# Kernel optimization log

Hardware: AMD Instinct MI355X
Metric: run time of the kernel (lower is better)

Reference implementation:

```python
import jax, jax.numpy as jnp
import numpy as np

ALPHA = 0.2  # LeakyReLU negative slope
NEG = -9e15

def _gat_head(Wh, a1, a2, adj_mask):
    # Wh: [N,O], a1/a2: [O], adj_mask: [N,N] bool
    e = jax.nn.leaky_relu(jnp.einsum('no,o->n', Wh, a1)[:, None]
                          + jnp.einsum('no,o->n', Wh, a2)[None, :], ALPHA)
    att = jax.nn.softmax(jnp.where(adj_mask, e, NEG), axis=-1)
    return att @ Wh  # [N,O]

def setup_inputs() -> dict:
    key = jax.random.key(0)
    ks = jax.random.split(key, 6)
    N, F_IN, O, H, C = 4096, 512, 64, 8, 16
    x = jax.random.normal(ks[0], (N, F_IN), jnp.float32)
    adj = jax.random.randint(ks[1], (N, N), 0, 2, jnp.int32)
    W = jax.random.normal(ks[2], (H, F_IN, O), jnp.float32) * 0.05
    a = jax.random.normal(ks[3], (H, 2 * O), jnp.float32) * 0.05
    W_out = jax.random.normal(ks[4], (H * O, C), jnp.float32) * 0.05
    a_out = jax.random.normal(ks[5], (2 * C,), jnp.float32) * 0.05
    return {'x': x, 'adj': adj, 'W': W, 'a': a, 'W_out': W_out, 'a_out': a_out}

def reference(x, adj, W, a, W_out, a_out):
    N = x.shape[0]
    H, _, O = W.shape
    C = W_out.shape[1]
    mask = adj > 0  # [N,N]
    # multi-head attention layer (vmapped over heads)
    Wh = jnp.einsum('nf,hfo->hno', x, W)  # [H,N,O]
    a1, a2 = a[:, :O], a[:, O:]
    h_heads = jax.vmap(_gat_head, in_axes=(0, 0, 0, None))(Wh, a1, a2, mask)  # [H,N,O]
    h = jax.nn.elu(h_heads)  # concat=True -> elu per head
    h = jnp.transpose(h, (1, 0, 2)).reshape(N, H * O)  # concat heads
    # output attention layer (concat=False)
    Wh_o = h @ W_out  # [N,C]
    out = _gat_head(Wh_o, a_out[:C], a_out[C:], mask)  # [N,C]
    out = jax.nn.elu(out)
    return jax.nn.log_softmax(out, axis=1)
```

## Files before the change

kernel.cpp:

```cpp
#include <hip/hip_runtime.h>


typedef __attribute__((ext_vector_type(8))) short short8;
typedef __attribute__((ext_vector_type(4))) float f32x4;
typedef unsigned long long u64;
typedef unsigned short u16;
typedef unsigned int u32;

__device__ __forceinline__ u16 f2bf_rne(float f){
  u32 u = __float_as_uint(f);
  return (u16)((u + 0x7fffu + ((u >> 16) & 1u)) >> 16);
}
__device__ __forceinline__ void async16(void* lds, const void* g){
  __builtin_amdgcn_global_load_lds((const __attribute__((address_space(1))) u32*)g,
                                   (__attribute__((address_space(3))) u32*)lds, 16, 0, 0);
}
__device__ __forceinline__ void async4(void* lds, const void* g){
  __builtin_amdgcn_global_load_lds((const __attribute__((address_space(1))) u32*)g,
                                   (__attribute__((address_space(3))) u32*)lds, 4, 0, 0);
}

__global__ __launch_bounds__(256) void k_prep(const float* __restrict__ x,
                                              const float* __restrict__ W,
                                              const int* __restrict__ adj,
                                              u16* __restrict__ xA,
                                              u16* __restrict__ wB,
                                              u64* __restrict__ bits_t){
  int lane = threadIdx.x & 63;
  if (blockIdx.x < 1024){
    int t = blockIdx.x * 256 + threadIdx.x;
    int n = t & 4095, fg = t >> 12;
    const float* src = x + (size_t)n * 512 + fg * 8;
    float4 v0 = ((const float4*)src)[0];
    float4 v1 = ((const float4*)src)[1];
    u32 pk[4];
    pk[0] = f2bf_rne(v0.x) | ((u32)f2bf_rne(v0.y) << 16);
    pk[1] = f2bf_rne(v0.z) | ((u32)f2bf_rne(v0.w) << 16);
    pk[2] = f2bf_rne(v1.x) | ((u32)f2bf_rne(v1.y) << 16);
    pk[3] = f2bf_rne(v1.z) | ((u32)f2bf_rne(v1.w) << 16);
    *(uint4*)(xA + ((size_t)fg * 4096 + n) * 8) = *(uint4*)pk;
  } else if (blockIdx.x < 1152){
    int t = (blockIdx.x - 1024) * 256 + threadIdx.x;
    int o = t & 63, fg = (t >> 6) & 63, h = t >> 12;
    const float* src = W + ((size_t)h * 512 + fg * 8) * 64 + o;
    u32 pk[4];
    #pragma unroll
    for (int p = 0; p < 4; ++p){
      u16 lo = f2bf_rne(src[(2 * p) * 64]);
      u16 hi = f2bf_rne(src[(2 * p + 1) * 64]);
      pk[p] = lo | ((u32)hi << 16);
    }
    *(uint4*)(wB + (size_t)h * 32768 + ((size_t)fg * 64 + o) * 8) = *(uint4*)pk;
  } else {
    int Wd = (blockIdx.x - 1152) * 4 + (threadIdx.x >> 6);
    int jg = Wd >> 5;
    int i0 = (Wd & 31) * 128;
    const int* base = adj + (size_t)jg * 64 + lane;
    #pragma unroll 1
    for (int u = 0; u < 32; ++u){
      int ib = i0 + u * 4;
      int v0 = base[(size_t)(ib + 0) * 4096];
      int v1 = base[(size_t)(ib + 1) * 4096];
      int v2 = base[(size_t)(ib + 2) * 4096];
      int v3 = base[(size_t)(ib + 3) * 4096];
      u64 m0 = __ballot(v0 != 0);
      u64 m1 = __ballot(v1 != 0);
      u64 m2 = __ballot(v2 != 0);
      u64 m3 = __ballot(v3 != 0);
      if (lane == 0){
        u64* d = bits_t + (size_t)jg * 4096 + ib;
        d[0] = m0; d[1] = m1; d[2] = m2; d[3] = m3;
      }
    }
  }
}

__global__ __launch_bounds__(256) void k_gemm1(const u16* __restrict__ xA,
                                               const u16* __restrict__ wB,
                                               const float* __restrict__ av,
                                               u16* __restrict__ whB,
                                               float* __restrict__ e11, float* __restrict__ e102,
                                               float* __restrict__ e21, float* __restrict__ e202){
  __shared__ u16 tr[4096];
  int h    = blockIdx.y;
  int nblk = blockIdx.x;
  int lane = threadIdx.x & 63;
  int wv   = threadIdx.x >> 6;
  int row16 = lane & 15, grp = lane >> 4;
  int n0 = nblk * 64;
  int n0w = n0 + wv * 16;
  const u16* wBh = wB + (size_t)h * 32768;
  f32x4 acc[4] = {};
  #pragma unroll 4
  for (int ks = 0; ks < 16; ++ks){
    int fgb = ks * 4 + grp;
    short8 af = *(const short8*)(xA + ((size_t)fgb * 4096 + n0w + row16) * 8);
    #pragma unroll
    for (int nt = 0; nt < 4; ++nt){
      short8 bf = *(const short8*)(wBh + ((size_t)fgb * 64 + nt * 16 + row16) * 8);
      acc[nt] = __builtin_amdgcn_mfma_f32_16x16x32_bf16(af, bf, acc[nt], 0, 0, 0);
    }
  }
  float a1v[4], a2v[4];
  #pragma unroll
  for (int nt = 0; nt < 4; ++nt){
    a1v[nt] = av[h * 128 + nt * 16 + row16];
    a2v[nt] = av[h * 128 + 64 + nt * 16 + row16];
  }
  #pragma unroll
  for (int r = 0; r < 4; ++r){
    float p1 = acc[0][r]*a1v[0] + acc[1][r]*a1v[1] + acc[2][r]*a1v[2] + acc[3][r]*a1v[3];
    float p2 = acc[0][r]*a2v[0] + acc[1][r]*a2v[1] + acc[2][r]*a2v[2] + acc[3][r]*a2v[3];
    #pragma unroll
    for (int d = 1; d < 16; d <<= 1){ p1 += __shfl_xor(p1, d, 64); p2 += __shfl_xor(p2, d, 64); }
    if (row16 == 0){
      int idx = h * 4096 + n0w + grp * 4 + r;
      e11[idx] = __expf(p1); e102[idx] = __expf(0.2f * p1);
      e21[idx] = __expf(p2); e202[idx] = __expf(0.2f * p2);
    }
  }
  #pragma unroll
  for (int nt = 0; nt < 4; ++nt)
    #pragma unroll
    for (int r = 0; r < 4; ++r){
      int jl = wv * 16 + grp * 4 + r;
      int o  = nt * 16 + row16;
      tr[((jl >> 3) * 64 + o) * 8 + (jl & 7)] = f2bf_rne(acc[nt][r]);
    }
  __syncthreads();
  u16* dst = whB + (size_t)h * 262144 + (size_t)n0 * 64;
  #pragma unroll
  for (int q = 0; q < 2; ++q)
    *(uint4*)(dst + (threadIdx.x * 2 + q) * 8) = *(const uint4*)(tr + (threadIdx.x * 2 + q) * 8);
}

__global__ __launch_bounds__(256) void k_att1(const u16* __restrict__ whB,
                                              const u64* __restrict__ bits_t,
                                              const float* __restrict__ e11, const float* __restrict__ e102,
                                              const float* __restrict__ e21, const float* __restrict__ e202,
                                              u16* __restrict__ pnum, float* __restrict__ pden){
  __shared__ u16  smB[2][4096];
  __shared__ float smT[2][2][64];
  __shared__ u32  smLut[4];
  int h     = blockIdx.y;
  int iblk  = blockIdx.x;
  int split = blockIdx.z;
  int lane = threadIdx.x & 63;
  int wv   = threadIdx.x >> 6;
  int row16 = lane & 15, grp = lane >> 4;
  if (threadIdx.x < 4)
    smLut[threadIdx.x] = ((threadIdx.x & 1) ? 0xFFFFu : 0u) | ((threadIdx.x & 2) ? 0xFFFF0000u : 0u);
  int i = iblk * 64 + wv * 16 + row16;
  int hoff = h * 4096;
  float f1  = e11[hoff + i];
  float f02 = e102[hoff + i];
  const u16* whBh = whB + (size_t)h * 262144;
  int jbeg = split * 1024;

  short8 bden;
  #pragma unroll
  for (int t = 0; t < 8; ++t) bden[t] = (row16 == 0) ? (short)0x3F80 : (short)0;

  auto stage = [&](int bb, int j0){
    const char* g = (const char*)whBh + (size_t)j0 * 128 + wv * 2048 + lane * 16;
    char* l = (char*)(&smB[bb][0]) + wv * 2048;
    async16(l, g);
    async16(l + 1024, g + 1024);
    if (wv == 0)      async4(&smT[bb][0][0], (const char*)(e21  + hoff + j0) + lane * 4);
    else if (wv == 1) async4(&smT[bb][1][0], (const char*)(e202 + hoff + j0) + lane * 4);
  };

  f32x4 acc[4] = {};
  f32x4 accden = {};
  stage(0, jbeg);
  for (int c = 0; c < 16; ++c){
    int bb = c & 1;
    u64 mrow = bits_t[(size_t)(split * 16 + c) * 4096 + i];
    __syncthreads();
    if (c < 15) stage(bb ^ 1, jbeg + (c + 1) * 64);
    #pragma unroll
    for (int ks = 0; ks < 2; ++ks){
      int kb = ks * 32 + grp * 8;
      float4 eA = *(const float4*)(&smT[bb][0][kb]);
      float4 eB = *(const float4*)(&smT[bb][0][kb + 4]);
      float4 gA = *(const float4*)(&smT[bb][1][kb]);
      float4 gB = *(const float4*)(&smT[bb][1][kb + 4]);
      float e1v[8] = {eA.x, eA.y, eA.z, eA.w, eB.x, eB.y, eB.z, eB.w};
      float e2v[8] = {gA.x, gA.y, gA.z, gA.w, gB.x, gB.y, gB.z, gB.w};
      const u16* bbase = &smB[bb][(ks * 4 + grp) * 512];
      short8 bf0 = *(const short8*)(bbase + (0 * 16 + row16) * 8);
      short8 bf1 = *(const short8*)(bbase + (1 * 16 + row16) * 8);
      short8 bf2 = *(const short8*)(bbase + (2 * 16 + row16) * 8);
      short8 bf3 = *(const short8*)(bbase + (3 * 16 + row16) * 8);
      u32 mb = ((u32)(mrow >> (ks * 32)) >> (grp * 8)) & 0xffu;
      u32 pk[4];
      #pragma unroll
      for (int t2i = 0; t2i < 4; ++t2i){
        float w0 = fmaxf(f1 * e1v[2 * t2i],     f02 * e2v[2 * t2i]);
        float w1 = fmaxf(f1 * e1v[2 * t2i + 1], f02 * e2v[2 * t2i + 1]);
        u32 p = __builtin_amdgcn_perm(__float_as_uint(w1), __float_as_uint(w0), 0x07060302u);
        pk[t2i] = p & smLut[(mb >> (2 * t2i)) & 3u];
      }
      short8 af = *(short8*)pk;
      acc[0] = __builtin_amdgcn_mfma_f32_16x16x32_bf16(af, bf0, acc[0], 0, 0, 0);
      acc[1] = __builtin_amdgcn_mfma_f32_16x16x32_bf16(af, bf1, acc[1], 0, 0, 0);
      acc[2] = __builtin_amdgcn_mfma_f32_16x16x32_bf16(af, bf2, acc[2], 0, 0, 0);
      acc[3] = __builtin_amdgcn_mfma_f32_16x16x32_bf16(af, bf3, acc[3], 0, 0, 0);
      accden = __builtin_amdgcn_mfma_f32_16x16x32_bf16(af, bden, accden, 0, 0, 0);
    }
  }

  #pragma unroll
  for (int r = 0; r < 4; ++r){
    int n = iblk * 64 + wv * 16 + grp * 4 + r;
    if (row16 == 0)
      pden[((size_t)split * 8 + h) * 4096 + n] = accden[r];
    u16* dst = pnum + ((size_t)split * 4096 + n) * 512 + h * 64 + row16;
    #pragma unroll
    for (int nt = 0; nt < 4; ++nt)
      dst[nt * 16] = f2bf_rne(acc[nt][r]);
  }
}

__global__ __launch_bounds__(256) void k_gemm2(const u16* __restrict__ pnum,
                                               const float* __restrict__ pden,
                                               const float* __restrict__ Wout,
                                               const float* __restrict__ aout,
                                               u16* __restrict__ whoB,
                                               float* __restrict__ e11o, float* __restrict__ e102o,
                                               float* __restrict__ e21o, float* __restrict__ e202o){
  __shared__ float Wl[8192];
  __shared__ float hrow[16 * 516];
  __shared__ float sden[128];
  int n0 = blockIdx.x * 16;
  for (int t = threadIdx.x; t < 8192; t += 256) Wl[t] = Wout[t];
  if (threadIdx.x < 128){
    int hh = threadIdx.x >> 4, nn = threadIdx.x & 15;
    float d = 0.f;
    #pragma unroll
    for (int s = 0; s < 4; ++s) d += pden[((size_t)s * 8 + hh) * 4096 + n0 + nn];
    sden[threadIdx.x] = d;
  }
  __syncthreads();
  {
    int nn = threadIdx.x >> 4;
    int fc = threadIdx.x & 15;
    int f0 = fc * 32;
    int hh = fc >> 1;
    float dinv = 1.f / sden[hh * 16 + nn];
    float v[32];
    #pragma unroll
    for (int k = 0; k < 32; ++k) v[k] = 0.f;
    #pragma unroll
    for (int s = 0; s < 4; ++s){
      const u16* p = pnum + ((size_t)s * 4096 + n0 + nn) * 512 + f0;
      #pragma unroll
      for (int q = 0; q < 4; ++q){
        uint4 raw = *(const uint4*)(p + q * 8);
        u32 rw[4] = {raw.x, raw.y, raw.z, raw.w};
        #pragma unroll
        for (int d2 = 0; d2 < 4; ++d2){
          v[q * 8 + d2 * 2]     += __uint_as_float(rw[d2] << 16);
          v[q * 8 + d2 * 2 + 1] += __uint_as_float(rw[d2] & 0xffff0000u);
        }
      }
    }
    #pragma unroll
    for (int k = 0; k < 32; ++k){
      float val = v[k] * dinv;
      val = val > 0.f ? val : (__expf(val) - 1.f);
      hrow[nn * 516 + f0 + k] = val;
    }
  }
  __syncthreads();
  int c  = threadIdx.x & 15;
  int rl = threadIdx.x >> 4;
  int n = n0 + rl;
  const float4* hr = (const float4*)(hrow + rl * 516);
  float acc = 0.f;
  #pragma unroll 8
  for (int f4 = 0; f4 < 128; ++f4){
    float4 hv = hr[f4];
    int f = f4 * 4;
    acc += hv.x * Wl[f * 16 + c] + hv.y * Wl[(f + 1) * 16 + c]
         + hv.z * Wl[(f + 2) * 16 + c] + hv.w * Wl[(f + 3) * 16 + c];
  }
  whoB[((size_t)(n >> 3) * 16 + c) * 8 + (n & 7)] = f2bf_rne(acc);
  float p1 = acc * aout[c], p2 = acc * aout[16 + c];
  #pragma unroll
  for (int d = 1; d < 16; d <<= 1){ p1 += __shfl_xor(p1, d, 64); p2 += __shfl_xor(p2, d, 64); }
  if (c == 0){
    e11o[n] = __expf(p1); e102o[n] = __expf(0.2f * p1);
    e21o[n] = __expf(p2); e202o[n] = __expf(0.2f * p2);
  }
}

__global__ __launch_bounds__(256) void k_att2(const u16* __restrict__ whoB,
                                              const u64* __restrict__ bits_t,
                                              const float* __restrict__ e11o, const float* __restrict__ e102o,
                                              const float* __restrict__ e21o, const float* __restrict__ e202o,
                                              float* __restrict__ pnum, float* __restrict__ pden){
  __shared__ u32 smLut[4];
  int iblk  = blockIdx.x;
  int split = blockIdx.y;
  int lane = threadIdx.x & 63;
  int wv   = threadIdx.x >> 6;
  int row16 = lane & 15, grp = lane >> 4;
  if (threadIdx.x < 4)
    smLut[threadIdx.x] = ((threadIdx.x & 1) ? 0xFFFFu : 0u) | ((threadIdx.x & 2) ? 0xFFFF0000u : 0u);
  __syncthreads();
  int i = iblk * 64 + wv * 16 + row16;
  float f1  = e11o[i];
  float f02 = e102o[i];
  int jbeg = split * 256;
  short8 bden;
  #pragma unroll
  for (int t = 0; t < 8; ++t) bden[t] = (row16 == 0) ? (short)0x3F80 : (short)0;

  f32x4 acc = {};
  f32x4 accden = {};
  #pragma unroll
  for (int c = 0; c < 4; ++c){
    int j0 = jbeg + c * 64;
    u64 mrow = bits_t[(size_t)(split * 4 + c) * 4096 + i];
    #pragma unroll
    for (int ks = 0; ks < 2; ++ks){
      int sb = (j0 >> 3) + ks * 4 + grp;
      short8 bf = *(const short8*)(whoB + ((size_t)sb * 16 + row16) * 8);
      const float* t1 = e21o  + j0 + ks * 32 + grp * 8;
      const float* t2 = e202o + j0 + ks * 32 + grp * 8;
      float4 eA = *(const float4*)t1;
      float4 eB = *(const float4*)(t1 + 4);
      float4 gA = *(const float4*)t2;
      float4 gB = *(const float4*)(t2 + 4);
      float e1v[8] = {eA.x, eA.y, eA.z, eA.w, eB.x, eB.y, eB.z, eB.w};
      float e2v[8] = {gA.x, gA.y, gA.z, gA.w, gB.x, gB.y, gB.z, gB.w};
      u32 mb = ((u32)(mrow >> (ks * 32)) >> (grp * 8)) & 0xffu;
      u32 pk[4];
      #pragma unroll
      for (int t2i = 0; t2i < 4; ++t2i){
        float w0 = fmaxf(f1 * e1v[2 * t2i],     f02 * e2v[2 * t2i]);
        float w1 = fmaxf(f1 * e1v[2 * t2i + 1], f02 * e2v[2 * t2i + 1]);
        u32 p = __builtin_amdgcn_perm(__float_as_uint(w1), __float_as_uint(w0), 0x07060302u);
        pk[t2i] = p & smLut[(mb >> (2 * t2i)) & 3u];
      }
      short8 af = *(short8*)pk;
      acc    = __builtin_amdgcn_mfma_f32_16x16x32_bf16(af, bf, acc, 0, 0, 0);
      accden = __builtin_amdgcn_mfma_f32_16x16x32_bf16(af, bden, accden, 0, 0, 0);
    }
  }
  #pragma unroll
  for (int r = 0; r < 4; ++r){
    int n = iblk * 64 + wv * 16 + grp * 4 + r;
    if (row16 == 0)
      pden[(size_t)n * 16 + split] = accden[r];
    pnum[((size_t)n * 16 + split) * 16 + row16] = acc[r];
  }
}

__global__ __launch_bounds__(256) void k_final(const float* __restrict__ pnum,
                                               const float* __restrict__ pden,
                                               float* __restrict__ out){
  int tid = blockIdx.x * 256 + threadIdx.x;
  int c = tid & 15;
  int n = tid >> 4;
  float num = 0.f, den = 0.f;
  #pragma unroll
  for (int s = 0; s < 16; ++s){
    num += pnum[((size_t)n * 16 + s) * 16 + c];
    den += pden[(size_t)n * 16 + s];
  }
  float v = num / den;
  v = v > 0.f ? v : (__expf(v) - 1.f);
  float m = v;
  #pragma unroll
  for (int d = 1; d < 16; d <<= 1) m = fmaxf(m, __shfl_xor(m, d, 64));
  float es = __expf(v - m), ss = es;
  #pragma unroll
  for (int d = 1; d < 16; d <<= 1) ss += __shfl_xor(ss, d, 64);
  out[(size_t)n * 16 + c] = v - m - __logf(ss);
}

extern "C" void kernel_launch(void* const* d_in, const int* in_sizes, int n_in,
                              void* d_out, int out_size, void* d_ws, size_t ws_size,
                              hipStream_t stream){
  (void)in_sizes; (void)n_in; (void)out_size; (void)ws_size;
  const float* x    = (const float*)d_in[0];
  const int*   adj  = (const int*)d_in[1];
  const float* W    = (const float*)d_in[2];
  const float* av   = (const float*)d_in[3];
  const float* Wout = (const float*)d_in[4];
  const float* aout = (const float*)d_in[5];
  float* out = (float*)d_out;
  char* ws = (char*)d_ws;

  u64*  bits_t  = (u64*)(ws + 0x0000000);
  u16*  whB     = (u16*)(ws + 0x0200000);
  float* e11    = (float*)(ws + 0x0600000);
  float* e102   = (float*)(ws + 0x0620000);
  float* e21    = (float*)(ws + 0x0640000);
  float* e202   = (float*)(ws + 0x0660000);
  u16*  xA      = (u16*)(ws + 0x0680000);
  u16*  wB      = (u16*)(ws + 0x0A80000);
  u16*  pnum1   = (u16*)(ws + 0x0680000);
  float* pden1  = (float*)(ws + 0x1680000);
  u16*  whoB    = (u16*)(ws + 0x1700000);
  float* e11o   = (float*)(ws + 0x1720000);
  float* e102o  = (float*)(ws + 0x1724000);
  float* e21o   = (float*)(ws + 0x1728000);
  float* e202o  = (float*)(ws + 0x172C000);
  float* pnum2  = (float*)(ws + 0x1730000);
  float* pden2  = (float*)(ws + 0x1B30000);

  k_prep<<<dim3(1664), dim3(256), 0, stream>>>(x, W, adj, xA, wB, bits_t);
  k_gemm1<<<dim3(64, 8), dim3(256), 0, stream>>>(xA, wB, av, whB, e11, e102, e21, e202);
  k_att1<<<dim3(64, 8, 4), dim3(256), 0, stream>>>(whB, bits_t, e11, e102, e21, e202, pnum1, pden1);
  k_gemm2<<<dim3(256), dim3(256), 0, stream>>>(pnum1, pden1, Wout, aout, whoB, e11o, e102o, e21o, e202o);
  k_att2<<<dim3(64, 16), dim3(256), 0, stream>>>(whoB, bits_t, e11o, e102o, e21o, e202o, pnum2, pden2);
  k_final<<<dim3(256), dim3(256), 0, stream>>>(pnum2, pden2, out);
}
```

Measured before the change: 191.7 us.

## Fuse prep/gemm1 and gemm2/att2/final into persistent kernels with grid barriers

Merges the prep and first projection GEMM into one 1024-block kernel, and the second projection, output attention and final log-softmax into another. The stages are separated by a software two-level atomic grid barrier, which replaces five launches with two plus a memset. The adjacency bit-packing is remapped so that each wave reads contiguous rows. gemm2 now runs on 4 rows per block with a split-K reduction and reads Wout from global memory instead of LDS. The grid barrier depends on all 1024 blocks being co-resident (launch_bounds 256,4 over 256 CUs), so the code can deadlock if occupancy falls short.

```diff
diff --git a/kernel.cpp b/kernel.cpp
--- a/kernel.cpp
+++ b/kernel.cpp
@@ -20,15 +20,50 @@
                                    (__attribute__((address_space(3))) u32*)lds, 4, 0, 0);
 }
 
-__global__ __launch_bounds__(256) void k_prep(const float* __restrict__ x,
-                                              const float* __restrict__ W,
-                                              const int* __restrict__ adj,
-                                              u16* __restrict__ xA,
-                                              u16* __restrict__ wB,
-                                              u64* __restrict__ bits_t){
-  int lane = threadIdx.x & 63;
-  if (blockIdx.x < 1024){
-    int t = blockIdx.x * 256 + threadIdx.x;
+__device__ __forceinline__ void grid_barrier(u32* bar){
+  __syncthreads();
+  if (threadIdx.x == 0){
+    u32* gen  = bar;
+    u32* root = bar + 32;
+    u32* leaf = bar + 64 + (blockIdx.x & 31) * 32;
+    u32 mygen = __hip_atomic_load(gen, __ATOMIC_RELAXED, __HIP_MEMORY_SCOPE_AGENT);
+    __threadfence();
+    u32 o = __hip_atomic_fetch_add(leaf, 1u, __ATOMIC_RELAXED, __HIP_MEMORY_SCOPE_AGENT);
+    if (o == 31u){
+      __hip_atomic_store(leaf, 0u, __ATOMIC_RELAXED, __HIP_MEMORY_SCOPE_AGENT);
+      u32 r = __hip_atomic_fetch_add(root, 1u, __ATOMIC_RELAXED, __HIP_MEMORY_SCOPE_AGENT);
+      if (r == 31u){
+        __hip_atomic_store(root, 0u, __ATOMIC_RELAXED, __HIP_MEMORY_SCOPE_AGENT);
+        __threadfence();
+        __hip_atomic_fetch_add(gen, 1u, __ATOMIC_RELEASE, __HIP_MEMORY_SCOPE_AGENT);
+      } else {
+        while (__hip_atomic_load(gen, __ATOMIC_RELAXED, __HIP_MEMORY_SCOPE_AGENT) == mygen)
+          __builtin_amdgcn_s_sleep(16);
+      }
+    } else {
+      while (__hip_atomic_load(gen, __ATOMIC_RELAXED, __HIP_MEMORY_SCOPE_AGENT) == mygen)
+        __builtin_amdgcn_s_sleep(16);
+    }
+    __threadfence();
+  }
+  __syncthreads();
+}
+
+__global__ __launch_bounds__(256, 4) void k_gat_a(
+    const float* __restrict__ x, const float* __restrict__ W,
+    const int* __restrict__ adj, const float* __restrict__ av,
+    u16* __restrict__ xA, u16* __restrict__ wB, u64* __restrict__ bits_t,
+    u16* __restrict__ whB,
+    float* __restrict__ e11, float* __restrict__ e102,
+    float* __restrict__ e21, float* __restrict__ e202, u32* bar)
+{
+  __shared__ u16 tr[4096];
+  const int tid = threadIdx.x, b = blockIdx.x;
+  const int lane = tid & 63, wv = tid >> 6;
+  const int row16 = lane & 15, grp = lane >> 4;
+
+  {
+    int t = b * 256 + tid;
     int n = t & 4095, fg = t >> 12;
     const float* src = x + (size_t)n * 512 + fg * 8;
     float4 v0 = ((const float4*)src)[0];
@@ -39,8 +74,9 @@
     pk[2] = f2bf_rne(v1.x) | ((u32)f2bf_rne(v1.y) << 16);
     pk[3] = f2bf_rne(v1.z) | ((u32)f2bf_rne(v1.w) << 16);
     *(uint4*)(xA + ((size_t)fg * 4096 + n) * 8) = *(uint4*)pk;
-  } else if (blockIdx.x < 1152){
-    int t = (blockIdx.x - 1024) * 256 + threadIdx.x;
+  }
+  if (b < 128){
+    int t = b * 256 + tid;
     int o = t & 63, fg = (t >> 6) & 63, h = t >> 12;
     const float* src = W + ((size_t)h * 512 + fg * 8) * 64 + o;
     u32 pk[4];
@@ -51,87 +87,67 @@
       pk[p] = lo | ((u32)hi << 16);
     }
     *(uint4*)(wB + (size_t)h * 32768 + ((size_t)fg * 64 + o) * 8) = *(uint4*)pk;
-  } else {
-    int Wd = (blockIdx.x - 1152) * 4 + (threadIdx.x >> 6);
-    int jg = Wd >> 5;
-    int i0 = (Wd & 31) * 128;
-    const int* base = adj + (size_t)jg * 64 + lane;
-    #pragma unroll 1
-    for (int u = 0; u < 32; ++u){
-      int ib = i0 + u * 4;
-      int v0 = base[(size_t)(ib + 0) * 4096];
-      int v1 = base[(size_t)(ib + 1) * 4096];
-      int v2 = base[(size_t)(ib + 2) * 4096];
-      int v3 = base[(size_t)(ib + 3) * 4096];
-      u64 m0 = __ballot(v0 != 0);
-      u64 m1 = __ballot(v1 != 0);
-      u64 m2 = __ballot(v2 != 0);
-      u64 m3 = __ballot(v3 != 0);
-      if (lane == 0){
-        u64* d = bits_t + (size_t)jg * 4096 + ib;
-        d[0] = m0; d[1] = m1; d[2] = m2; d[3] = m3;
-      }
-    }
-  }
-}
-
-__global__ __launch_bounds__(256) void k_gemm1(const u16* __restrict__ xA,
-                                               const u16* __restrict__ wB,
-                                               const float* __restrict__ av,
-                                               u16* __restrict__ whB,
-                                               float* __restrict__ e11, float* __restrict__ e102,
-                                               float* __restrict__ e21, float* __restrict__ e202){
-  __shared__ u16 tr[4096];
-  int h    = blockIdx.y;
-  int nblk = blockIdx.x;
-  int lane = threadIdx.x & 63;
-  int wv   = threadIdx.x >> 6;
-  int row16 = lane & 15, grp = lane >> 4;
-  int n0 = nblk * 64;
-  int n0w = n0 + wv * 16;
-  const u16* wBh = wB + (size_t)h * 32768;
-  f32x4 acc[4] = {};
-  #pragma unroll 4
-  for (int ks = 0; ks < 16; ++ks){
-    int fgb = ks * 4 + grp;
-    short8 af = *(const short8*)(xA + ((size_t)fgb * 4096 + n0w + row16) * 8);
+  }
+  {
+    int w = b * 4 + wv;
+    #pragma unroll 4
+    for (int k = 0; k < 64; ++k){
+      int uid = w + k * 4096;
+      int i = uid >> 6, jg = uid & 63;
+      int v = adj[(size_t)i * 4096 + (jg << 6) + lane];
+      u64 m = __ballot(v != 0);
+      if (lane == 0) bits_t[(size_t)jg * 4096 + i] = m;
+    }
+  }
+  grid_barrier(bar);
+
+  if (b < 512){
+    int h = b >> 6, nblk = b & 63;
+    int n0 = nblk * 64, n0w = n0 + wv * 16;
+    const u16* wBh = wB + (size_t)h * 32768;
+    f32x4 acc[4] = {};
+    #pragma unroll 4
+    for (int ks = 0; ks < 16; ++ks){
+      int fgb = ks * 4 + grp;
+      short8 af = *(const short8*)(xA + ((size_t)fgb * 4096 + n0w + row16) * 8);
+      #pragma unroll
+      for (int nt = 0; nt < 4; ++nt){
+        short8 bf = *(const short8*)(wBh + ((size_t)fgb * 64 + nt * 16 + row16) * 8);
+        acc[nt] = __builtin_amdgcn_mfma_f32_16x16x32_bf16(af, bf, acc[nt], 0, 0, 0);
+      }
+    }
+    float a1v[4], a2v[4];
     #pragma unroll
     for (int nt = 0; nt < 4; ++nt){
-      short8 bf = *(const short8*)(wBh + ((size_t)fgb * 64 + nt * 16 + row16) * 8);
-      acc[nt] = __builtin_amdgcn_mfma_f32_16x16x32_bf16(af, bf, acc[nt], 0, 0, 0);
-    }
-  }
-  float a1v[4], a2v[4];
-  #pragma unroll
-  for (int nt = 0; nt < 4; ++nt){
-    a1v[nt] = av[h * 128 + nt * 16 + row16];
-    a2v[nt] = av[h * 128 + 64 + nt * 16 + row16];
-  }
-  #pragma unroll
-  for (int r = 0; r < 4; ++r){
-    float p1 = acc[0][r]*a1v[0] + acc[1][r]*a1v[1] + acc[2][r]*a1v[2] + acc[3][r]*a1v[3];
-    float p2 = acc[0][r]*a2v[0] + acc[1][r]*a2v[1] + acc[2][r]*a2v[2] + acc[3][r]*a2v[3];
-    #pragma unroll
-    for (int d = 1; d < 16; d <<= 1){ p1 += __shfl_xor(p1, d, 64); p2 += __shfl_xor(p2, d, 64); }
-    if (row16 == 0){
-      int idx = h * 4096 + n0w + grp * 4 + r;
-      e11[idx] = __expf(p1); e102[idx] = __expf(0.2f * p1);
-      e21[idx] = __expf(p2); e202[idx] = __expf(0.2f * p2);
-    }
-  }
-  #pragma unroll
-  for (int nt = 0; nt < 4; ++nt)
+      a1v[nt] = av[h * 128 + nt * 16 + row16];
+      a2v[nt] = av[h * 128 + 64 + nt * 16 + row16];
+    }
     #pragma unroll
     for (int r = 0; r < 4; ++r){
-      int jl = wv * 16 + grp * 4 + r;
-      int o  = nt * 16 + row16;
-      tr[((jl >> 3) * 64 + o) * 8 + (jl & 7)] = f2bf_rne(acc[nt][r]);
-    }
-  __syncthreads();
-  u16* dst = whB + (size_t)h * 262144 + (size_t)n0 * 64;
-  #pragma unroll
-  for (int q = 0; q < 2; ++q)
-    *(uint4*)(dst + (threadIdx.x * 2 + q) * 8) = *(const uint4*)(tr + (threadIdx.x * 2 + q) * 8);
+      float p1 = acc[0][r]*a1v[0] + acc[1][r]*a1v[1] + acc[2][r]*a1v[2] + acc[3][r]*a1v[3];
+      float p2 = acc[0][r]*a2v[0] + acc[1][r]*a2v[1] + acc[2][r]*a2v[2] + acc[3][r]*a2v[3];
+      #pragma unroll
+      for (int d = 1; d < 16; d <<= 1){ p1 += __shfl_xor(p1, d, 64); p2 += __shfl_xor(p2, d, 64); }
+      if (row16 == 0){
+        int idx = h * 4096 + n0w + grp * 4 + r;
+        e11[idx] = __expf(p1); e102[idx] = __expf(0.2f * p1);
+        e21[idx] = __expf(p2); e202[idx] = __expf(0.2f * p2);
+      }
+    }
+    #pragma unroll
+    for (int nt = 0; nt < 4; ++nt)
+      #pragma unroll
+      for (int r = 0; r < 4; ++r){
+        int jl = wv * 16 + grp * 4 + r;
+        int o  = nt * 16 + row16;
+        tr[((jl >> 3) * 64 + o) * 8 + (jl & 7)] = f2bf_rne(acc[nt][r]);
+      }
+    __syncthreads();
+    u16* dst = whB + (size_t)h * 262144 + (size_t)n0 * 64;
+    #pragma unroll
+    for (int q = 0; q < 2; ++q)
+      *(uint4*)(dst + (tid * 2 + q) * 8) = *(const uint4*)(tr + (tid * 2 + q) * 8);
+  }
 }
 
 __global__ __launch_bounds__(256) void k_att1(const u16* __restrict__ whB,
@@ -222,163 +238,162 @@
   }
 }
 
-__global__ __launch_bounds__(256) void k_gemm2(const u16* __restrict__ pnum,
-                                               const float* __restrict__ pden,
-                                               const float* __restrict__ Wout,
-                                               const float* __restrict__ aout,
-                                               u16* __restrict__ whoB,
-                                               float* __restrict__ e11o, float* __restrict__ e102o,
-                                               float* __restrict__ e21o, float* __restrict__ e202o){
-  __shared__ float Wl[8192];
-  __shared__ float hrow[16 * 516];
-  __shared__ float sden[128];
-  int n0 = blockIdx.x * 16;
-  for (int t = threadIdx.x; t < 8192; t += 256) Wl[t] = Wout[t];
-  if (threadIdx.x < 128){
-    int hh = threadIdx.x >> 4, nn = threadIdx.x & 15;
-    float d = 0.f;
-    #pragma unroll
-    for (int s = 0; s < 4; ++s) d += pden[((size_t)s * 8 + hh) * 4096 + n0 + nn];
-    sden[threadIdx.x] = d;
-  }
-  __syncthreads();
+__global__ __launch_bounds__(256, 4) void k_gat_c(
+    const u16* __restrict__ pnum1, const float* __restrict__ pden1,
+    const float* __restrict__ Wout, const float* __restrict__ aout,
+    const u64* __restrict__ bits_t,
+    u16* __restrict__ whoB,
+    float* __restrict__ e11o, float* __restrict__ e102o,
+    float* __restrict__ e21o, float* __restrict__ e202o,
+    float* __restrict__ pnum2, float* __restrict__ pden2,
+    float* __restrict__ out, u32* bar)
+{
+  __shared__ __align__(16) char smem[10496];
+  float* s_hrow = (float*)smem;
+  float* s_red  = (float*)(smem + 8320);
+  float* s_den  = (float*)(smem + 9344);
+  u32*   s_lut  = (u32*)(smem + 10240);
+  const int tid = threadIdx.x, b = blockIdx.x;
+  const int lane = tid & 63, wv = tid >> 6;
+  const int row16 = lane & 15, grp = lane >> 4;
+
+  if (tid < 4)
+    s_lut[tid] = ((tid & 1) ? 0xFFFFu : 0u) | ((tid & 2) ? 0xFFFF0000u : 0u);
+
   {
-    int nn = threadIdx.x >> 4;
-    int fc = threadIdx.x & 15;
-    int f0 = fc * 32;
-    int hh = fc >> 1;
-    float dinv = 1.f / sden[hh * 16 + nn];
-    float v[32];
-    #pragma unroll
-    for (int k = 0; k < 32; ++k) v[k] = 0.f;
-    #pragma unroll
-    for (int s = 0; s < 4; ++s){
-      const u16* p = pnum + ((size_t)s * 4096 + n0 + nn) * 512 + f0;
-      #pragma unroll
-      for (int q = 0; q < 4; ++q){
-        uint4 raw = *(const uint4*)(p + q * 8);
+    int n0 = b * 4;
+    if (tid < 32){
+      int hh = tid >> 2, nn = tid & 3;
+      float d = 0.f;
+      #pragma unroll
+      for (int s = 0; s < 4; ++s) d += pden1[((size_t)s * 8 + hh) * 4096 + n0 + nn];
+      s_den[tid] = d;
+    }
+    __syncthreads();
+    {
+      int nn = tid >> 6;
+      int fo = (tid & 63) * 8;
+      int hh = fo >> 6;
+      float dinv = 1.f / s_den[hh * 4 + nn];
+      float v[8] = {0.f,0.f,0.f,0.f,0.f,0.f,0.f,0.f};
+      #pragma unroll
+      for (int s = 0; s < 4; ++s){
+        uint4 raw = *(const uint4*)(pnum1 + ((size_t)s * 4096 + n0 + nn) * 512 + fo);
         u32 rw[4] = {raw.x, raw.y, raw.z, raw.w};
         #pragma unroll
         for (int d2 = 0; d2 < 4; ++d2){
-          v[q * 8 + d2 * 2]     += __uint_as_float(rw[d2] << 16);
-          v[q * 8 + d2 * 2 + 1] += __uint_as_float(rw[d2] & 0xffff0000u);
+          v[d2 * 2]     += __uint_as_float(rw[d2] << 16);
+          v[d2 * 2 + 1] += __uint_as_float(rw[d2] & 0xffff0000u);
         }
       }
-    }
-    #pragma unroll
-    for (int k = 0; k < 32; ++k){
-      float val = v[k] * dinv;
-      val = val > 0.f ? val : (__expf(val) - 1.f);
-      hrow[nn * 516 + f0 + k] = val;
-    }
-  }
-  __syncthreads();
-  int c  = threadIdx.x & 15;
-  int rl = threadIdx.x >> 4;
-  int n = n0 + rl;
-  const float4* hr = (const float4*)(hrow + rl * 516);
-  float acc = 0.f;
-  #pragma unroll 8
-  for (int f4 = 0; f4 < 128; ++f4){
-    float4 hv = hr[f4];
-    int f = f4 * 4;
-    acc += hv.x * Wl[f * 16 + c] + hv.y * Wl[(f + 1) * 16 + c]
-         + hv.z * Wl[(f + 2) * 16 + c] + hv.w * Wl[(f + 3) * 16 + c];
-  }
-  whoB[((size_t)(n >> 3) * 16 + c) * 8 + (n & 7)] = f2bf_rne(acc);
-  float p1 = acc * aout[c], p2 = acc * aout[16 + c];
-  #pragma unroll
-  for (int d = 1; d < 16; d <<= 1){ p1 += __shfl_xor(p1, d, 64); p2 += __shfl_xor(p2, d, 64); }
-  if (c == 0){
-    e11o[n] = __expf(p1); e102o[n] = __expf(0.2f * p1);
-    e21o[n] = __expf(p2); e202o[n] = __expf(0.2f * p2);
-  }
-}
-
-__global__ __launch_bounds__(256) void k_att2(const u16* __restrict__ whoB,
-                                              const u64* __restrict__ bits_t,
-                                              const float* __restrict__ e11o, const float* __restrict__ e102o,
-                                              const float* __restrict__ e21o, const float* __restrict__ e202o,
-                                              float* __restrict__ pnum, float* __restrict__ pden){
-  __shared__ u32 smLut[4];
-  int iblk  = blockIdx.x;
-  int split = blockIdx.y;
-  int lane = threadIdx.x & 63;
-  int wv   = threadIdx.x >> 6;
-  int row16 = lane & 15, grp = lane >> 4;
-  if (threadIdx.x < 4)
-    smLut[threadIdx.x] = ((threadIdx.x & 1) ? 0xFFFFu : 0u) | ((threadIdx.x & 2) ? 0xFFFF0000u : 0u);
-  __syncthreads();
-  int i = iblk * 64 + wv * 16 + row16;
-  float f1  = e11o[i];
-  float f02 = e102o[i];
-  int jbeg = split * 256;
-  short8 bden;
-  #pragma unroll
-  for (int t = 0; t < 8; ++t) bden[t] = (row16 == 0) ? (short)0x3F80 : (short)0;
-
-  f32x4 acc = {};
-  f32x4 accden = {};
-  #pragma unroll
-  for (int c = 0; c < 4; ++c){
-    int j0 = jbeg + c * 64;
-    u64 mrow = bits_t[(size_t)(split * 4 + c) * 4096 + i];
-    #pragma unroll
-    for (int ks = 0; ks < 2; ++ks){
-      int sb = (j0 >> 3) + ks * 4 + grp;
-      short8 bf = *(const short8*)(whoB + ((size_t)sb * 16 + row16) * 8);
-      const float* t1 = e21o  + j0 + ks * 32 + grp * 8;
-      const float* t2 = e202o + j0 + ks * 32 + grp * 8;
-      float4 eA = *(const float4*)t1;
-      float4 eB = *(const float4*)(t1 + 4);
-      float4 gA = *(const float4*)t2;
-      float4 gB = *(const float4*)(t2 + 4);
-      float e1v[8] = {eA.x, eA.y, eA.z, eA.w, eB.x, eB.y, eB.z, eB.w};
-      float e2v[8] = {gA.x, gA.y, gA.z, gA.w, gB.x, gB.y, gB.z, gB.w};
-      u32 mb = ((u32)(mrow >> (ks * 32)) >> (grp * 8)) & 0xffu;
-      u32 pk[4];
-      #pragma unroll
-      for (int t2i = 0; t2i < 4; ++t2i){
-        float w0 = fmaxf(f1 * e1v[2 * t2i],     f02 * e2v[2 * t2i]);
-        float w1 = fmaxf(f1 * e1v[2 * t2i + 1], f02 * e2v[2 * t2i + 1]);
-        u32 p = __builtin_amdgcn_perm(__float_as_uint(w1), __float_as_uint(w0), 0x07060302u);
-        pk[t2i] = p & smLut[(mb >> (2 * t2i)) & 3u];
-      }
-      short8 af = *(short8*)pk;
-      acc    = __builtin_amdgcn_mfma_f32_16x16x32_bf16(af, bf, acc, 0, 0, 0);
-      accden = __builtin_amdgcn_mfma_f32_16x16x32_bf16(af, bden, accden, 0, 0, 0);
-    }
-  }
-  #pragma unroll
-  for (int r = 0; r < 4; ++r){
-    int n = iblk * 64 + wv * 16 + grp * 4 + r;
-    if (row16 == 0)
-      pden[(size_t)n * 16 + split] = accden[r];
-    pnum[((size_t)n * 16 + split) * 16 + row16] = acc[r];
-  }
-}
-
-__global__ __launch_bounds__(256) void k_final(const float* __restrict__ pnum,
-                                               const float* __restrict__ pden,
-                                               float* __restrict__ out){
-  int tid = blockIdx.x * 256 + threadIdx.x;
-  int c = tid & 15;
-  int n = tid >> 4;
-  float num = 0.f, den = 0.f;
-  #pragma unroll
-  for (int s = 0; s < 16; ++s){
-    num += pnum[((size_t)n * 16 + s) * 16 + c];
-    den += pden[(size_t)n * 16 + s];
-  }
-  float v = num / den;
-  v = v > 0.f ? v : (__expf(v) - 1.f);
-  float m = v;
-  #pragma unroll
-  for (int d = 1; d < 16; d <<= 1) m = fmaxf(m, __shfl_xor(m, d, 64));
-  float es = __expf(v - m), ss = es;
-  #pragma unroll
-  for (int d = 1; d < 16; d <<= 1) ss += __shfl_xor(ss, d, 64);
-  out[(size_t)n * 16 + c] = v - m - __logf(ss);
+      #pragma unroll
+      for (int j = 0; j < 8; ++j){
+        float val = v[j] * dinv;
+        val = val > 0.f ? val : (__expf(val) - 1.f);
+        s_hrow[nn * 520 + fo + j] = val;
+      }
+    }
+    __syncthreads();
+    {
+      int c = tid & 15, rl = (tid >> 4) & 3, ks = tid >> 6;
+      float acc = 0.f;
+      #pragma unroll 8
+      for (int f4 = 0; f4 < 32; ++f4){
+        int f = ks * 128 + f4 * 4;
+        float4 hv = *(const float4*)(s_hrow + rl * 520 + f);
+        acc += hv.x * Wout[f * 16 + c] + hv.y * Wout[(f + 1) * 16 + c]
+             + hv.z * Wout[(f + 2) * 16 + c] + hv.w * Wout[(f + 3) * 16 + c];
+      }
+      s_red[tid] = acc;
+      __syncthreads();
+      if (tid < 64){
+        float total = acc + s_red[tid + 64] + s_red[tid + 128] + s_red[tid + 192];
+        int n = n0 + rl;
+        whoB[((size_t)(n >> 3) * 16 + c) * 8 + (n & 7)] = f2bf_rne(total);
+        float p1 = total * aout[c], p2 = total * aout[16 + c];
+        #pragma unroll
+        for (int d = 1; d < 16; d <<= 1){ p1 += __shfl_xor(p1, d, 64); p2 += __shfl_xor(p2, d, 64); }
+        if (c == 0){
+          e11o[n] = __expf(p1); e102o[n] = __expf(0.2f * p1);
+          e21o[n] = __expf(p2); e202o[n] = __expf(0.2f * p2);
+        }
+      }
+    }
+  }
+  grid_barrier(bar);
+
+  {
+    int split = b >> 6, iblk = b & 63;
+    int i = iblk * 64 + wv * 16 + row16;
+    float f1  = e11o[i];
+    float f02 = e102o[i];
+    int jbeg = split * 256;
+    short8 bden;
+    #pragma unroll
+    for (int t = 0; t < 8; ++t) bden[t] = (row16 == 0) ? (short)0x3F80 : (short)0;
+
+    f32x4 acc = {};
+    f32x4 accden = {};
+    #pragma unroll
+    for (int c = 0; c < 4; ++c){
+      int j0 = jbeg + c * 64;
+      u64 mrow = bits_t[(size_t)(split * 4 + c) * 4096 + i];
+      #pragma unroll
+      for (int ks = 0; ks < 2; ++ks){
+        int sb = (j0 >> 3) + ks * 4 + grp;
+        short8 bf = *(const short8*)(whoB + ((size_t)sb * 16 + row16) * 8);
+        const float* t1 = e21o  + j0 + ks * 32 + grp * 8;
+        const float* t2 = e202o + j0 + ks * 32 + grp * 8;
+        float4 eA = *(const float4*)t1;
+        float4 eB = *(const float4*)(t1 + 4);
+        float4 gA = *(const float4*)t2;
+        float4 gB = *(const float4*)(t2 + 4);
+        float e1v[8] = {eA.x, eA.y, eA.z, eA.w, eB.x, eB.y, eB.z, eB.w};
+        float e2v[8] = {gA.x, gA.y, gA.z, gA.w, gB.x, gB.y, gB.z, gB.w};
+        u32 mb = ((u32)(mrow >> (ks * 32)) >> (grp * 8)) & 0xffu;
+        u32 pk[4];
+        #pragma unroll
+        for (int t2i = 0; t2i < 4; ++t2i){
+          float w0 = fmaxf(f1 * e1v[2 * t2i],     f02 * e2v[2 * t2i]);
+          float w1 = fmaxf(f1 * e1v[2 * t2i + 1], f02 * e2v[2 * t2i + 1]);
+          u32 p = __builtin_amdgcn_perm(__float_as_uint(w1), __float_as_uint(w0), 0x07060302u);
+          pk[t2i] = p & s_lut[(mb >> (2 * t2i)) & 3u];
+        }
+        short8 af = *(short8*)pk;
+        acc    = __builtin_amdgcn_mfma_f32_16x16x32_bf16(af, bf, acc, 0, 0, 0);
+        accden = __builtin_amdgcn_mfma_f32_16x16x32_bf16(af, bden, accden, 0, 0, 0);
+      }
+    }
+    #pragma unroll
+    for (int r = 0; r < 4; ++r){
+      int n = iblk * 64 + wv * 16 + grp * 4 + r;
+      if (row16 == 0)
+        pden2[(size_t)n * 16 + split] = accden[r];
+      pnum2[((size_t)n * 16 + split) * 16 + row16] = acc[r];
+    }
+  }
+  grid_barrier(bar);
+
+  if (b < 256){
+    int t = b * 256 + tid;
+    int c = t & 15;
+    int n = t >> 4;
+    float num = 0.f, den = 0.f;
+    #pragma unroll
+    for (int s = 0; s < 16; ++s){
+      num += pnum2[((size_t)n * 16 + s) * 16 + c];
+      den += pden2[(size_t)n * 16 + s];
+    }
+    float v = num / den;
+    v = v > 0.f ? v : (__expf(v) - 1.f);
+    float m = v;
+    #pragma unroll
+    for (int d = 1; d < 16; d <<= 1) m = fmaxf(m, __shfl_xor(m, d, 64));
+    float es = __expf(v - m), ss = es;
+    #pragma unroll
+    for (int d = 1; d < 16; d <<= 1) ss += __shfl_xor(ss, d, 64);
+    out[(size_t)n * 16 + c] = v - m - __logf(ss);
+  }
 }
 
 extern "C" void kernel_launch(void* const* d_in, const int* in_sizes, int n_in,
@@ -411,11 +426,16 @@
   float* e202o  = (float*)(ws + 0x172C000);
   float* pnum2  = (float*)(ws + 0x1730000);
   float* pden2  = (float*)(ws + 0x1B30000);
-
-  k_prep<<<dim3(1664), dim3(256), 0, stream>>>(x, W, adj, xA, wB, bits_t);
-  k_gemm1<<<dim3(64, 8), dim3(256), 0, stream>>>(xA, wB, av, whB, e11, e102, e21, e202);
-  k_att1<<<dim3(64, 8, 4), dim3(256), 0, stream>>>(whB, bits_t, e11, e102, e21, e202, pnum1, pden1);
-  k_gemm2<<<dim3(256), dim3(256), 0, stream>>>(pnum1, pden1, Wout, aout, whoB, e11o, e102o, e21o, e202o);
-  k_att2<<<dim3(64, 16), dim3(256), 0, stream>>>(whoB, bits_t, e11o, e102o, e21o, e202o, pnum2, pden2);
-  k_final<<<dim3(256), dim3(256), 0, stream>>>(pnum2, pden2, out);
-}
+  u32*  barA    = (u32*)(ws + 0x1C00000);
+  u32*  barC    = (u32*)(ws + 0x1C02000);
+
+  hipMemsetAsync(ws + 0x1C00000, 0, 16384, stream);
+
+  k_gat_a<<<dim3(1024), dim3(256), 0, stream>>>(x, W, adj, av, xA, wB, bits_t,
+                                                whB, e11, e102, e21, e202, barA);
+  k_att1<<<dim3(64, 8, 4), dim3(256), 0, stream>>>(whB, bits_t, e11, e102, e21, e202,
+                                                   pnum1, pden1);
+  k_gat_c<<<dim3(1024), dim3(256), 0, stream>>>(pnum1, pden1, Wout, aout, bits_t,
+                                                whoB, e11o, e102o, e21o, e202o,
+                                                pnum2, pden2, out, barC);
+}
```

New measurement: 327.8 us. +71.0%, slower.

## Fuse adjacency bitpacking into gemm1, simplify attention weights, merge att2 with final

Applied to the files above, without the earlier changes.

Moves the adjacency-to-bitmask packing out of the prep kernel and into the tail of k_gemm1. Rewrites the LeakyReLU exponent weights so each row uses a single factor exp(-0.8*p1) instead of two, which drops one multiply per element. k_att1 now reads the per-column e2 values straight from global memory instead of staging them through LDS. k_att2 and k_final are fused into one kernel that reduces the split partials in shared memory, removing the pnum2/pden2 round trip and one launch. Dividing the weights by a per-row constant cancels in the softmax, but it can change overflow behaviour, and the adjacency pass in gemm1 reads with a different access pattern.

```diff
diff --git a/kernel.cpp b/kernel.cpp
--- a/kernel.cpp
+++ b/kernel.cpp
@@ -15,18 +15,11 @@
   __builtin_amdgcn_global_load_lds((const __attribute__((address_space(1))) u32*)g,
                                    (__attribute__((address_space(3))) u32*)lds, 16, 0, 0);
 }
-__device__ __forceinline__ void async4(void* lds, const void* g){
-  __builtin_amdgcn_global_load_lds((const __attribute__((address_space(1))) u32*)g,
-                                   (__attribute__((address_space(3))) u32*)lds, 4, 0, 0);
-}
 
 __global__ __launch_bounds__(256) void k_prep(const float* __restrict__ x,
                                               const float* __restrict__ W,
-                                              const int* __restrict__ adj,
                                               u16* __restrict__ xA,
-                                              u16* __restrict__ wB,
-                                              u64* __restrict__ bits_t){
-  int lane = threadIdx.x & 63;
+                                              u16* __restrict__ wB){
   if (blockIdx.x < 1024){
     int t = blockIdx.x * 256 + threadIdx.x;
     int n = t & 4095, fg = t >> 12;
@@ -39,7 +32,7 @@
     pk[2] = f2bf_rne(v1.x) | ((u32)f2bf_rne(v1.y) << 16);
     pk[3] = f2bf_rne(v1.z) | ((u32)f2bf_rne(v1.w) << 16);
     *(uint4*)(xA + ((size_t)fg * 4096 + n) * 8) = *(uint4*)pk;
-  } else if (blockIdx.x < 1152){
+  } else {
     int t = (blockIdx.x - 1024) * 256 + threadIdx.x;
     int o = t & 63, fg = (t >> 6) & 63, h = t >> 12;
     const float* src = W + ((size_t)h * 512 + fg * 8) * 64 + o;
@@ -51,35 +44,16 @@
       pk[p] = lo | ((u32)hi << 16);
     }
     *(uint4*)(wB + (size_t)h * 32768 + ((size_t)fg * 64 + o) * 8) = *(uint4*)pk;
-  } else {
-    int Wd = (blockIdx.x - 1152) * 4 + (threadIdx.x >> 6);
-    int jg = Wd >> 5;
-    int i0 = (Wd & 31) * 128;
-    const int* base = adj + (size_t)jg * 64 + lane;
-    #pragma unroll 1
-    for (int u = 0; u < 32; ++u){
-      int ib = i0 + u * 4;
-      int v0 = base[(size_t)(ib + 0) * 4096];
-      int v1 = base[(size_t)(ib + 1) * 4096];
-      int v2 = base[(size_t)(ib + 2) * 4096];
-      int v3 = base[(size_t)(ib + 3) * 4096];
-      u64 m0 = __ballot(v0 != 0);
-      u64 m1 = __ballot(v1 != 0);
-      u64 m2 = __ballot(v2 != 0);
-      u64 m3 = __ballot(v3 != 0);
-      if (lane == 0){
-        u64* d = bits_t + (size_t)jg * 4096 + ib;
-        d[0] = m0; d[1] = m1; d[2] = m2; d[3] = m3;
-      }
-    }
   }
 }
 
 __global__ __launch_bounds__(256) void k_gemm1(const u16* __restrict__ xA,
                                                const u16* __restrict__ wB,
                                                const float* __restrict__ av,
+                                               const int* __restrict__ adj,
                                                u16* __restrict__ whB,
-                                               float* __restrict__ e11, float* __restrict__ e102,
+                                               u64* __restrict__ bits_t,
+                                               float* __restrict__ r1,
                                                float* __restrict__ e21, float* __restrict__ e202){
   __shared__ u16 tr[4096];
   int h    = blockIdx.y;
@@ -115,8 +89,9 @@
     for (int d = 1; d < 16; d <<= 1){ p1 += __shfl_xor(p1, d, 64); p2 += __shfl_xor(p2, d, 64); }
     if (row16 == 0){
       int idx = h * 4096 + n0w + grp * 4 + r;
-      e11[idx] = __expf(p1); e102[idx] = __expf(0.2f * p1);
-      e21[idx] = __expf(p2); e202[idx] = __expf(0.2f * p2);
+      r1[idx]   = __expf(-0.8f * p1);
+      e21[idx]  = __expf(p2);
+      e202[idx] = __expf(0.2f * p2);
     }
   }
   #pragma unroll
@@ -132,15 +107,37 @@
   #pragma unroll
   for (int q = 0; q < 2; ++q)
     *(uint4*)(dst + (threadIdx.x * 2 + q) * 8) = *(const uint4*)(tr + (threadIdx.x * 2 + q) * 8);
+
+  {
+    int B = blockIdx.y * 64 + blockIdx.x;
+    int uid0 = B * 512 + wv * 128;
+    for (int k = 0; k < 128; k += 8){
+      int v[8];
+      #pragma unroll
+      for (int q = 0; q < 8; ++q){
+        int uid = uid0 + k + q;
+        v[q] = adj[(size_t)(uid >> 6) * 4096 + ((uid & 63) << 6) + lane];
+      }
+      u64 m[8];
+      #pragma unroll
+      for (int q = 0; q < 8; ++q) m[q] = __ballot(v[q] != 0);
+      if (lane == 0){
+        #pragma unroll
+        for (int q = 0; q < 8; ++q){
+          int uid = uid0 + k + q;
+          bits_t[(size_t)(uid & 63) * 4096 + (uid >> 6)] = m[q];
+        }
+      }
+    }
+  }
 }
 
 __global__ __launch_bounds__(256) void k_att1(const u16* __restrict__ whB,
                                               const u64* __restrict__ bits_t,
-                                              const float* __restrict__ e11, const float* __restrict__ e102,
+                                              const float* __restrict__ r1,
                                               const float* __restrict__ e21, const float* __restrict__ e202,
                                               u16* __restrict__ pnum, float* __restrict__ pden){
   __shared__ u16  smB[2][4096];
-  __shared__ float smT[2][2][64];
   __shared__ u32  smLut[4];
   int h     = blockIdx.y;
   int iblk  = blockIdx.x;
@@ -152,8 +149,7 @@
     smLut[threadIdx.x] = ((threadIdx.x & 1) ? 0xFFFFu : 0u) | ((threadIdx.x & 2) ? 0xFFFF0000u : 0u);
   int i = iblk * 64 + wv * 16 + row16;
   int hoff = h * 4096;
-  float f1  = e11[hoff + i];
-  float f02 = e102[hoff + i];
+  float r = r1[hoff + i];
   const u16* whBh = whB + (size_t)h * 262144;
   int jbeg = split * 1024;
 
@@ -166,8 +162,6 @@
     char* l = (char*)(&smB[bb][0]) + wv * 2048;
     async16(l, g);
     async16(l + 1024, g + 1024);
-    if (wv == 0)      async4(&smT[bb][0][0], (const char*)(e21  + hoff + j0) + lane * 4);
-    else if (wv == 1) async4(&smT[bb][1][0], (const char*)(e202 + hoff + j0) + lane * 4);
   };
 
   f32x4 acc[4] = {};
@@ -175,16 +169,18 @@
   stage(0, jbeg);
   for (int c = 0; c < 16; ++c){
     int bb = c & 1;
+    int j0 = jbeg + c * 64;
     u64 mrow = bits_t[(size_t)(split * 16 + c) * 4096 + i];
     __syncthreads();
-    if (c < 15) stage(bb ^ 1, jbeg + (c + 1) * 64);
+    if (c < 15) stage(bb ^ 1, j0 + 64);
     #pragma unroll
     for (int ks = 0; ks < 2; ++ks){
-      int kb = ks * 32 + grp * 8;
-      float4 eA = *(const float4*)(&smT[bb][0][kb]);
-      float4 eB = *(const float4*)(&smT[bb][0][kb + 4]);
-      float4 gA = *(const float4*)(&smT[bb][1][kb]);
-      float4 gB = *(const float4*)(&smT[bb][1][kb + 4]);
+      const float* t1 = e21  + hoff + j0 + ks * 32 + grp * 8;
+      const float* t2 = e202 + hoff + j0 + ks * 32 + grp * 8;
+      float4 eA = *(const float4*)t1;
+      float4 eB = *(const float4*)(t1 + 4);
+      float4 gA = *(const float4*)t2;
+      float4 gB = *(const float4*)(t2 + 4);
       float e1v[8] = {eA.x, eA.y, eA.z, eA.w, eB.x, eB.y, eB.z, eB.w};
       float e2v[8] = {gA.x, gA.y, gA.z, gA.w, gB.x, gB.y, gB.z, gB.w};
       const u16* bbase = &smB[bb][(ks * 4 + grp) * 512];
@@ -196,8 +192,8 @@
       u32 pk[4];
       #pragma unroll
       for (int t2i = 0; t2i < 4; ++t2i){
-        float w0 = fmaxf(f1 * e1v[2 * t2i],     f02 * e2v[2 * t2i]);
-        float w1 = fmaxf(f1 * e1v[2 * t2i + 1], f02 * e2v[2 * t2i + 1]);
+        float w0 = fmaxf(e1v[2 * t2i],     r * e2v[2 * t2i]);
+        float w1 = fmaxf(e1v[2 * t2i + 1], r * e2v[2 * t2i + 1]);
         u32 p = __builtin_amdgcn_perm(__float_as_uint(w1), __float_as_uint(w0), 0x07060302u);
         pk[t2i] = p & smLut[(mb >> (2 * t2i)) & 3u];
       }
@@ -211,14 +207,14 @@
   }
 
   #pragma unroll
-  for (int r = 0; r < 4; ++r){
-    int n = iblk * 64 + wv * 16 + grp * 4 + r;
+  for (int r4 = 0; r4 < 4; ++r4){
+    int n = iblk * 64 + wv * 16 + grp * 4 + r4;
     if (row16 == 0)
-      pden[((size_t)split * 8 + h) * 4096 + n] = accden[r];
+      pden[((size_t)split * 8 + h) * 4096 + n] = accden[r4];
     u16* dst = pnum + ((size_t)split * 4096 + n) * 512 + h * 64 + row16;
     #pragma unroll
     for (int nt = 0; nt < 4; ++nt)
-      dst[nt * 16] = f2bf_rne(acc[nt][r]);
+      dst[nt * 16] = f2bf_rne(acc[nt][r4]);
   }
 }
 
@@ -227,7 +223,7 @@
                                                const float* __restrict__ Wout,
                                                const float* __restrict__ aout,
                                                u16* __restrict__ whoB,
-                                               float* __restrict__ e11o, float* __restrict__ e102o,
+                                               float* __restrict__ r1o,
                                                float* __restrict__ e21o, float* __restrict__ e202o){
   __shared__ float Wl[8192];
   __shared__ float hrow[16 * 516];
@@ -290,39 +286,39 @@
   #pragma unroll
   for (int d = 1; d < 16; d <<= 1){ p1 += __shfl_xor(p1, d, 64); p2 += __shfl_xor(p2, d, 64); }
   if (c == 0){
-    e11o[n] = __expf(p1); e102o[n] = __expf(0.2f * p1);
-    e21o[n] = __expf(p2); e202o[n] = __expf(0.2f * p2);
-  }
-}
-
-__global__ __launch_bounds__(256) void k_att2(const u16* __restrict__ whoB,
-                                              const u64* __restrict__ bits_t,
-                                              const float* __restrict__ e11o, const float* __restrict__ e102o,
-                                              const float* __restrict__ e21o, const float* __restrict__ e202o,
-                                              float* __restrict__ pnum, float* __restrict__ pden){
+    r1o[n]   = __expf(-0.8f * p1);
+    e21o[n]  = __expf(p2);
+    e202o[n] = __expf(0.2f * p2);
+  }
+}
+
+__global__ __launch_bounds__(256) void k_att2f(const u16* __restrict__ whoB,
+                                               const u64* __restrict__ bits_t,
+                                               const float* __restrict__ r1o,
+                                               const float* __restrict__ e21o, const float* __restrict__ e202o,
+                                               float* __restrict__ out){
+  __shared__ float s_acc[4][16][16];
+  __shared__ float s_den[4][16];
   __shared__ u32 smLut[4];
-  int iblk  = blockIdx.x;
-  int split = blockIdx.y;
-  int lane = threadIdx.x & 63;
-  int wv   = threadIdx.x >> 6;
+  int n0 = blockIdx.x * 16;
+  int tid = threadIdx.x;
+  int lane = tid & 63, wv = tid >> 6;
   int row16 = lane & 15, grp = lane >> 4;
-  if (threadIdx.x < 4)
-    smLut[threadIdx.x] = ((threadIdx.x & 1) ? 0xFFFFu : 0u) | ((threadIdx.x & 2) ? 0xFFFF0000u : 0u);
+  if (tid < 4)
+    smLut[tid] = ((tid & 1) ? 0xFFFFu : 0u) | ((tid & 2) ? 0xFFFF0000u : 0u);
   __syncthreads();
-  int i = iblk * 64 + wv * 16 + row16;
-  float f1  = e11o[i];
-  float f02 = e102o[i];
-  int jbeg = split * 256;
+  int i = n0 + row16;
+  float r = r1o[i];
   short8 bden;
   #pragma unroll
   for (int t = 0; t < 8; ++t) bden[t] = (row16 == 0) ? (short)0x3F80 : (short)0;
 
   f32x4 acc = {};
   f32x4 accden = {};
-  #pragma unroll
-  for (int c = 0; c < 4; ++c){
-    int j0 = jbeg + c * 64;
-    u64 mrow = bits_t[(size_t)(split * 4 + c) * 4096 + i];
+  int jbase = wv * 1024;
+  for (int c = 0; c < 16; ++c){
+    int j0 = jbase + c * 64;
+    u64 mrow = bits_t[(size_t)(wv * 16 + c) * 4096 + i];
     #pragma unroll
     for (int ks = 0; ks < 2; ++ks){
       int sb = (j0 >> 3) + ks * 4 + grp;
@@ -339,8 +335,8 @@
       u32 pk[4];
       #pragma unroll
       for (int t2i = 0; t2i < 4; ++t2i){
-        float w0 = fmaxf(f1 * e1v[2 * t2i],     f02 * e2v[2 * t2i]);
-        float w1 = fmaxf(f1 * e1v[2 * t2i + 1], f02 * e2v[2 * t2i + 1]);
+        float w0 = fmaxf(e1v[2 * t2i],     r * e2v[2 * t2i]);
+        float w1 = fmaxf(e1v[2 * t2i + 1], r * e2v[2 * t2i + 1]);
         u32 p = __builtin_amdgcn_perm(__float_as_uint(w1), __float_as_uint(w0), 0x07060302u);
         pk[t2i] = p & smLut[(mb >> (2 * t2i)) & 3u];
       }
@@ -350,35 +346,25 @@
     }
   }
   #pragma unroll
-  for (int r = 0; r < 4; ++r){
-    int n = iblk * 64 + wv * 16 + grp * 4 + r;
-    if (row16 == 0)
-      pden[(size_t)n * 16 + split] = accden[r];
-    pnum[((size_t)n * 16 + split) * 16 + row16] = acc[r];
-  }
-}
-
-__global__ __launch_bounds__(256) void k_final(const float* __restrict__ pnum,
-                                               const float* __restrict__ pden,
-                                               float* __restrict__ out){
-  int tid = blockIdx.x * 256 + threadIdx.x;
-  int c = tid & 15;
-  int n = tid >> 4;
-  float num = 0.f, den = 0.f;
-  #pragma unroll
-  for (int s = 0; s < 16; ++s){
-    num += pnum[((size_t)n * 16 + s) * 16 + c];
-    den += pden[(size_t)n * 16 + s];
-  }
-  float v = num / den;
-  v = v > 0.f ? v : (__expf(v) - 1.f);
-  float m = v;
-  #pragma unroll
-  for (int d = 1; d < 16; d <<= 1) m = fmaxf(m, __shfl_xor(m, d, 64));
-  float es = __expf(v - m), ss = es;
-  #pragma unroll
-  for (int d = 1; d < 16; d <<= 1) ss += __shfl_xor(ss, d, 64);
-  out[(size_t)n * 16 + c] = v - m - __logf(ss);
+  for (int r4 = 0; r4 < 4; ++r4){
+    s_acc[wv][grp * 4 + r4][row16] = acc[r4];
+    if (row16 == 0) s_den[wv][grp * 4 + r4] = accden[r4];
+  }
+  __syncthreads();
+  {
+    int row = tid >> 4, c = tid & 15;
+    float num = s_acc[0][row][c] + s_acc[1][row][c] + s_acc[2][row][c] + s_acc[3][row][c];
+    float den = s_den[0][row] + s_den[1][row] + s_den[2][row] + s_den[3][row];
+    float v = num / den;
+    v = v > 0.f ? v : (__expf(v) - 1.f);
+    float m = v;
+    #pragma unroll
+    for (int d = 1; d < 16; d <<= 1) m = fmaxf(m, __shfl_xor(m, d, 64));
+    float es = __expf(v - m), ss = es;
+    #pragma unroll
+    for (int d = 1; d < 16; d <<= 1) ss += __shfl_xor(ss, d, 64);
+    out[(size_t)(n0 + row) * 16 + c] = v - m - __logf(ss);
+  }
 }
 
 extern "C" void kernel_launch(void* const* d_in, const int* in_sizes, int n_in,
@@ -396,26 +382,21 @@
 
   u64*  bits_t  = (u64*)(ws + 0x0000000);
   u16*  whB     = (u16*)(ws + 0x0200000);
-  float* e11    = (float*)(ws + 0x0600000);
-  float* e102   = (float*)(ws + 0x0620000);
-  float* e21    = (float*)(ws + 0x0640000);
-  float* e202   = (float*)(ws + 0x0660000);
+  float* r1     = (float*)(ws + 0x0600000);
+  float* e21    = (float*)(ws + 0x0620000);
+  float* e202   = (float*)(ws + 0x0640000);
   u16*  xA      = (u16*)(ws + 0x0680000);
   u16*  wB      = (u16*)(ws + 0x0A80000);
   u16*  pnum1   = (u16*)(ws + 0x0680000);
   float* pden1  = (float*)(ws + 0x1680000);
   u16*  whoB    = (u16*)(ws + 0x1700000);
-  float* e11o   = (float*)(ws + 0x1720000);
-  float* e102o  = (float*)(ws + 0x1724000);
-  float* e21o   = (float*)(ws + 0x1728000);
-  float* e202o  = (float*)(ws + 0x172C000);
-  float* pnum2  = (float*)(ws + 0x1730000);
-  float* pden2  = (float*)(ws + 0x1B30000);
-
-  k_prep<<<dim3(1664), dim3(256), 0, stream>>>(x, W, adj, xA, wB, bits_t);
-  k_gemm1<<<dim3(64, 8), dim3(256), 0, stream>>>(xA, wB, av, whB, e11, e102, e21, e202);
-  k_att1<<<dim3(64, 8, 4), dim3(256), 0, stream>>>(whB, bits_t, e11, e102, e21, e202, pnum1, pden1);
-  k_gemm2<<<dim3(256), dim3(256), 0, stream>>>(pnum1, pden1, Wout, aout, whoB, e11o, e102o, e21o, e202o);
-  k_att2<<<dim3(64, 16), dim3(256), 0, stream>>>(whoB, bits_t, e11o, e102o, e21o, e202o, pnum2, pden2);
-  k_final<<<dim3(256), dim3(256), 0, stream>>>(pnum2, pden2, out);
-}
+  float* r1o    = (float*)(ws + 0x1720000);
+  float* e21o   = (float*)(ws + 0x1724000);
+  float* e202o  = (float*)(ws + 0x1728000);
+
+  k_prep<<<dim3(1152), dim3(256), 0, stream>>>(x, W, xA, wB);
+  k_gemm1<<<dim3(64, 8), dim3(256), 0, stream>>>(xA, wB, av, adj, whB, bits_t, r1, e21, e202);
+  k_att1<<<dim3(64, 8, 4), dim3(256), 0, stream>>>(whB, bits_t, r1, e21, e202, pnum1, pden1);
+  k_gemm2<<<dim3(256), dim3(256), 0, stream>>>(pnum1, pden1, Wout, aout, whoB, r1o, e21o, e202o);
+  k_att2f<<<dim3(256), dim3(256), 0, stream>>>(whoB, bits_t, r1o, e21o, e202o, out);
+}
```

Result: slower. 207.2 us (+8.1%).
